# Optimization experiments

Measured on AMD Instinct MI355X. Metric: run time of the kernel, lower is better.

The kernel has to match this reference:

```python
import jax, jax.numpy as jnp
import numpy as np

NUM_USERS = 100_000
NUM_ITEMS = 50_000
DIM = 64
N_INTERACTIONS = 2_000_000  # symmetric nnz = 4M


def setup_inputs() -> dict:
    rng = np.random.default_rng(0)
    u = rng.integers(0, NUM_USERS, N_INTERACTIONS)
    it = rng.integers(0, NUM_ITEMS, N_INTERACTIONS) + NUM_USERS  # items offset by num_users
    rows = np.concatenate([u, it]).astype(np.int32)  # symmetric adjacency
    cols = np.concatenate([it, u]).astype(np.int32)
    n_nodes = NUM_USERS + NUM_ITEMS
    deg = np.bincount(rows, minlength=n_nodes).astype(np.float32)
    deg = np.maximum(deg, 1.0)
    # LightGCN symmetric normalization: A_hat[i,j] = 1/sqrt(deg_i * deg_j)
    vals = (1.0 / np.sqrt(deg[rows] * deg[cols])).astype(np.float32)

    key = jax.random.key(0)
    k1, k2 = jax.random.split(key)
    user_emb = jax.random.normal(k1, (NUM_USERS, DIM), jnp.float32) * 0.1
    item_emb = jax.random.normal(k2, (NUM_ITEMS, DIM), jnp.float32) * 0.1
    return {
        "user_emb": user_emb,
        "item_emb": item_emb,
        "rows": jnp.asarray(rows),
        "cols": jnp.asarray(cols),
        "vals": jnp.asarray(vals),
        "n_layers": 3,
    }


def reference(user_emb, item_emb, rows, cols, vals, n_layers):
    num_users = user_emb.shape[0]
    n_nodes = num_users + item_emb.shape[0]
    emb = jnp.concatenate([user_emb, item_emb], axis=0)  # [N, D]
    acc = emb
    cur = emb
    for _ in range(n_layers):
        # SpMM: cur = A_hat @ cur, via edge gather + weighted segment reduction
        msgs = vals[:, None] * cur[cols]  # [nnz, D]
        cur = jax.ops.segment_sum(msgs, rows, num_segments=n_nodes)
        acc = acc + cur
    all_emb = acc / (n_layers + 1)  # mean over [e0, e1, ..., eL]
    return all_emb[:num_users], all_emb[num_users:]
```

## Files before the change

kernel.cpp:

```cpp
#include <hip/hip_runtime.h>
#include <hip/hip_fp16.h>

#define D 64
#define NLAYERS 3
#define CHUNK 8192
#define RPB 256
#define NBMAX 640
#define NCHMAX 512
#define STAGE_CAP 8704

typedef float vfloat4 __attribute__((ext_vector_type(4)));

__global__ void init_concat(const float* __restrict__ ue, const float* __restrict__ ie,
                            const float* __restrict__ invsq,
                            __half* __restrict__ w0,
                            int n_user_elems, int n_total_elems) {
    int i4 = (blockIdx.x * blockDim.x + threadIdx.x) * 4;
    if (i4 >= n_total_elems) return;
    float4 v;
    if (i4 < n_user_elems) v = *(const float4*)(ue + i4);
    else                   v = *(const float4*)(ie + (i4 - n_user_elems));
    float isr = invsq[i4 >> 6];
    __half2 h01 = __floats2half2_rn(isr * v.x, isr * v.y);
    __half2 h23 = __floats2half2_rn(isr * v.z, isr * v.w);
    float2 packed;
    *(__half2*)&packed.x = h01;
    *(__half2*)&packed.y = h23;
    *(float2*)(w0 + i4) = packed;
}

__global__ void partition_edges(const int* __restrict__ rows, const int* __restrict__ cols,
                                int* __restrict__ gsorted, int* __restrict__ goff_c,
                                int nnz, int nb) {
    __shared__ int staged[CHUNK];
    __shared__ int cnt[NBMAX];
    __shared__ int cur[NBMAX];
    __shared__ int partial[256];
    int t = threadIdx.x;
    int base = blockIdx.x * CHUNK;

    for (int j = t; j <= nb; j += 256) cnt[j] = 0;
    __syncthreads();
    for (int k = 0; k < CHUNK; k += 256) {
        int e = base + k + t;
        if (e < nnz) atomicAdd(&cnt[rows[e] >> 8], 1);
    }
    __syncthreads();
    int i0 = t * 3, i1 = i0 + 1, i2 = i0 + 2;
    int v0 = (i0 < nb) ? cnt[i0] : 0;
    int v1 = (i1 < nb) ? cnt[i1] : 0;
    int v2 = (i2 < nb) ? cnt[i2] : 0;
    partial[t] = v0 + v1 + v2;
    __syncthreads();
    for (int off = 1; off < 256; off <<= 1) {
        int x = (t >= off) ? partial[t - off] : 0;
        __syncthreads();
        partial[t] += x;
        __syncthreads();
    }
    int excl = (t == 0) ? 0 : partial[t - 1];
    if (i0 <= nb) cnt[i0] = excl;
    if (i1 <= nb) cnt[i1] = excl + v0;
    if (i2 <= nb) cnt[i2] = excl + v0 + v1;
    __syncthreads();
    for (int j = t; j < nb; j += 256) cur[j] = cnt[j];
    __syncthreads();
    for (int k = 0; k < CHUNK; k += 256) {
        int e = base + k + t;
        if (e < nnz) {
            int r = rows[e];
            int pos = atomicAdd(&cur[r >> 8], 1);
            staged[pos] = ((r & 255) << 18) | cols[e];
        }
    }
    __syncthreads();
    int total = cnt[nb];
    for (int i = t; i < total; i += 256) gsorted[base + i] = staged[i];
    for (int j = t; j <= nb; j += 256) goff_c[blockIdx.x * (nb + 1) + j] = cnt[j];
}

__global__ void transpose_off(const int* __restrict__ goff_c, int* __restrict__ T,
                              int nch, int nbp1) {
    int c = blockIdx.x * 256 + threadIdx.x;
    int j = blockIdx.y;
    if (c < nch) T[j * nch + c] = goff_c[c * nbp1 + j];
}

__global__ void bucket_totals(const int* __restrict__ T, int* __restrict__ btot, int nch) {
    int b = blockIdx.x;
    int lane = threadIdx.x;
    int s = 0;
    for (int c = lane; c < nch; c += 64)
        s += T[(size_t)(b + 1) * nch + c] - T[(size_t)b * nch + c];
    for (int off = 32; off; off >>= 1) s += __shfl_down(s, off, 64);
    if (lane == 0) btot[b] = s;
}

__global__ void scan_buckets(const int* __restrict__ btot, int* __restrict__ bb,
                             int* __restrict__ rp, int nb, int n_nodes, int nnz) {
    __shared__ int partial[256];
    int t = threadIdx.x;
    int i0 = t * 3, i1 = i0 + 1, i2 = i0 + 2;
    int v0 = (i0 < nb) ? btot[i0] : 0;
    int v1 = (i1 < nb) ? btot[i1] : 0;
    int v2 = (i2 < nb) ? btot[i2] : 0;
    partial[t] = v0 + v1 + v2;
    __syncthreads();
    for (int off = 1; off < 256; off <<= 1) {
        int x = (t >= off) ? partial[t - off] : 0;
        __syncthreads();
        partial[t] += x;
        __syncthreads();
    }
    int excl = (t == 0) ? 0 : partial[t - 1];
    if (i0 <= nb) bb[i0] = excl;
    if (i1 <= nb) bb[i1] = excl + v0;
    if (i2 <= nb) bb[i2] = excl + v0 + v1;
    if (t == 0) rp[n_nodes] = nnz;
}

__global__ __launch_bounds__(256)
void csr_build_bucket(const int* __restrict__ T, const int* __restrict__ gsorted,
                      const int* __restrict__ bb,
                      int* __restrict__ rp, float* __restrict__ invsq,
                      int* __restrict__ ci, int nch, int n_nodes) {
    __shared__ int staged[STAGE_CAP];
    __shared__ int sbeg[NCHMAX];
    __shared__ int slen[NCHMAX];
    __shared__ int soff[NCHMAX];
    __shared__ int cnt[RPB];
    __shared__ int cursor[RPB];
    __shared__ int scanb[256];
    int t = threadIdx.x;
    int b = blockIdx.x;
    for (int j = t; j < nch; j += 256) {
        int s0 = T[(size_t)b * nch + j];
        int s1 = T[(size_t)(b + 1) * nch + j];
        sbeg[j] = s0;
        slen[j] = s1 - s0;
    }
    cnt[t] = 0;
    __syncthreads();
    int i0 = 2 * t, i1 = 2 * t + 1;
    int l0 = (i0 < nch) ? slen[i0] : 0;
    int l1 = (i1 < nch) ? slen[i1] : 0;
    scanb[t] = l0 + l1;
    __syncthreads();
    for (int off = 1; off < 256; off <<= 1) {
        int x = (t >= off) ? scanb[t - off] : 0;
        __syncthreads();
        scanb[t] += x;
        __syncthreads();
    }
    int texcl = scanb[t] - (l0 + l1);
    if (i0 < nch) soff[i0] = texcl;
    if (i1 < nch) soff[i1] = texcl + l0;
    int total = scanb[255];
    __syncthreads();

    int w = t >> 6, lane = t & 63;
    int sub = lane >> 4, l16 = lane & 15;
    bool fits = (total <= STAGE_CAP);
    if (fits) {
        for (int c = (w << 2) + sub; c < nch; c += 16) {
            const int* seg = gsorted + (size_t)c * CHUNK + sbeg[c];
            int L = slen[c], o = soff[c];
            for (int i = l16; i < L; i += 16) staged[o + i] = seg[i];
        }
        __syncthreads();
        for (int i = t; i < total; i += 256) atomicAdd(&cnt[staged[i] >> 18], 1);
    } else {
        for (int c = (w << 2) + sub; c < nch; c += 16) {
            const int* seg = gsorted + (size_t)c * CHUNK + sbeg[c];
            int L = slen[c];
            for (int i = l16; i < L; i += 16) atomicAdd(&cnt[seg[i] >> 18], 1);
        }
    }
    __syncthreads();
    int v = cnt[t];
    scanb[t] = v;
    __syncthreads();
    for (int off = 1; off < 256; off <<= 1) {
        int x = (t >= off) ? scanb[t - off] : 0;
        __syncthreads();
        scanb[t] += x;
        __syncthreads();
    }
    int excl = scanb[t] - v;
    int base = bb[b];
    int grow = (b << 8) + t;
    if (grow < n_nodes) {
        rp[grow] = base + excl;
        float d = (float)v;
        invsq[grow] = rsqrtf(d < 1.f ? 1.f : d);
    }
    cursor[t] = base + excl;
    __syncthreads();
    if (fits) {
        for (int i = t; i < total; i += 256) {
            int p = staged[i];
            int pos = atomicAdd(&cursor[p >> 18], 1);
            ci[pos] = p & 0x3FFFF;
        }
    } else {
        for (int c = (w << 2) + sub; c < nch; c += 16) {
            const int* seg = gsorted + (size_t)c * CHUNK + sbeg[c];
            int L = slen[c];
            for (int i = l16; i < L; i += 16) {
                int p = seg[i];
                int pos = atomicAdd(&cursor[p >> 18], 1);
                ci[pos] = p & 0x3FFFF;
            }
        }
    }
}

__global__ __launch_bounds__(256)
void spmm_gather(const int* __restrict__ rp, const int* __restrict__ ci,
                 const __half* __restrict__ xh, const float* __restrict__ invsq,
                 __half* __restrict__ ynext,
                 const __half* __restrict__ opA,
                 const float* __restrict__ e0,
                 float* __restrict__ outp,
                 int row_beg, int row_end, int last) {
    int wid  = row_beg + ((blockIdx.x * blockDim.x + threadIdx.x) >> 6);
    int lane = threadIdx.x & 63;
    if (wid >= row_end) return;
    int sub = lane >> 4;
    int d4  = (lane & 15) << 2;
    int beg = rp[wid], end = rp[wid + 1];
    float isr = invsq[wid];

    float4 b4;
    float2 q1, q2;
    if (last && sub == 0) {
        size_t o = ((size_t)wid << 6) + d4;
        b4 = *(const float4*)(e0 + o);
        q1 = *(const float2*)(opA + o);
        q2 = *(const float2*)(xh + o);
    }

    __half2 z = __floats2half2_rn(0.f, 0.f);
    __half2 a01 = z, a23 = z, b01 = z, b23 = z;
    __half2 c01 = z, c23 = z, d01 = z, d23 = z;
    int e = beg + sub;
    for (; e + 12 < end; e += 16) {
        int k0 = __builtin_nontemporal_load(ci + e);
        int k1 = __builtin_nontemporal_load(ci + e + 4);
        int k2 = __builtin_nontemporal_load(ci + e + 8);
        int k3 = __builtin_nontemporal_load(ci + e + 12);
        float2 r0 = *(const float2*)(xh + ((size_t)k0 << 6) + d4);
        float2 r1 = *(const float2*)(xh + ((size_t)k1 << 6) + d4);
        float2 r2 = *(const float2*)(xh + ((size_t)k2 << 6) + d4);
        float2 r3 = *(const float2*)(xh + ((size_t)k3 << 6) + d4);
        a01 = __hadd2(a01, *(__half2*)&r0.x); a23 = __hadd2(a23, *(__half2*)&r0.y);
        b01 = __hadd2(b01, *(__half2*)&r1.x); b23 = __hadd2(b23, *(__half2*)&r1.y);
        c01 = __hadd2(c01, *(__half2*)&r2.x); c23 = __hadd2(c23, *(__half2*)&r2.y);
        d01 = __hadd2(d01, *(__half2*)&r3.x); d23 = __hadd2(d23, *(__half2*)&r3.y);
    }
    for (; e + 4 < end; e += 8) {
        int k0 = __builtin_nontemporal_load(ci + e);
        int k1 = __builtin_nontemporal_load(ci + e + 4);
        float2 r0 = *(const float2*)(xh + ((size_t)k0 << 6) + d4);
        float2 r1 = *(const float2*)(xh + ((size_t)k1 << 6) + d4);
        a01 = __hadd2(a01, *(__half2*)&r0.x); a23 = __hadd2(a23, *(__half2*)&r0.y);
        b01 = __hadd2(b01, *(__half2*)&r1.x); b23 = __hadd2(b23, *(__half2*)&r1.y);
    }
    if (e < end) {
        int k0 = ci[e];
        float2 r0 = *(const float2*)(xh + ((size_t)k0 << 6) + d4);
        a01 = __hadd2(a01, *(__half2*)&r0.x); a23 = __hadd2(a23, *(__half2*)&r0.y);
    }
    float2 fa = __half22float2(a01), fb = __half22float2(b01);
    float2 fc = __half22float2(c01), fd = __half22float2(d01);
    float sx = (fa.x + fb.x) + (fc.x + fd.x);
    float sy = (fa.y + fb.y) + (fc.y + fd.y);
    fa = __half22float2(a23); fb = __half22float2(b23);
    fc = __half22float2(c23); fd = __half22float2(d23);
    float sz = (fa.x + fb.x) + (fc.x + fd.x);
    float sw = (fa.y + fb.y) + (fc.y + fd.y);
    sx += __shfl_xor(sx, 16, 64); sy += __shfl_xor(sy, 16, 64);
    sz += __shfl_xor(sz, 16, 64); sw += __shfl_xor(sw, 16, 64);
    sx += __shfl_xor(sx, 32, 64); sy += __shfl_xor(sy, 32, 64);
    sz += __shfl_xor(sz, 32, 64); sw += __shfl_xor(sw, 32, 64);

    if (sub == 0) {
        size_t o = ((size_t)wid << 6) + d4;
        float cx = isr * sx, cy = isr * sy, cz = isr * sz, cw = isr * sw;
        if (last) {
            float sd = 1.0f / isr;
            float2 f1a = __half22float2(*(__half2*)&q1.x);
            float2 f1b = __half22float2(*(__half2*)&q1.y);
            float2 f2a = __half22float2(*(__half2*)&q2.x);
            float2 f2b = __half22float2(*(__half2*)&q2.y);
            vfloat4 o4;
            o4.x = (b4.x + (f1a.x + f2a.x) * sd + cx) * 0.25f;
            o4.y = (b4.y + (f1a.y + f2a.y) * sd + cy) * 0.25f;
            o4.z = (b4.z + (f1b.x + f2b.x) * sd + cz) * 0.25f;
            o4.w = (b4.w + (f1b.y + f2b.y) * sd + cw) * 0.25f;
            __builtin_nontemporal_store(o4, (vfloat4*)(outp + o));
        } else {
            __half2 h01 = __floats2half2_rn(isr * cx, isr * cy);
            __half2 h23 = __floats2half2_rn(isr * cz, isr * cw);
            float2 packed;
            *(__half2*)&packed.x = h01;
            *(__half2*)&packed.y = h23;
            *(float2*)(ynext + o) = packed;
        }
    }
}

extern "C" void kernel_launch(void* const* d_in, const int* in_sizes, int n_in,
                              void* d_out, int out_size, void* d_ws, size_t ws_size,
                              hipStream_t stream) {
    const float* ue   = (const float*)d_in[0];
    const float* ie   = (const float*)d_in[1];
    const int*   rows = (const int*)d_in[2];
    const int*   cols = (const int*)d_in[3];

    const int n_user_elems  = in_sizes[0];
    const int n_total_elems = out_size;
    const int n_nodes       = n_total_elems / D;
    const int n_user        = n_user_elems / D;
    const int nnz           = in_sizes[2];

    const int nb  = (n_nodes + RPB - 1) / RPB;
    const int nch = (nnz + CHUNK - 1) / CHUNK;

    float* out = (float*)d_out;

    char* w = (char*)d_ws;
    __half* w0h    = (__half*)w; w += (size_t)n_total_elems * 2;
    __half* w1h    = (__half*)w; w += (size_t)n_total_elems * 2;
    int*   gsorted = (int*)w;    w += (size_t)nch * CHUNK * 4;
    int*   ci      = (int*)w;    w += (size_t)nnz * 4;
    float* invsq   = (float*)w;  w += (size_t)n_nodes * 4;
    int*   rp      = (int*)w;    w += ((size_t)n_nodes + 16) * 4;
    int*   goff_c  = (int*)w;    w += (size_t)nch * (nb + 1) * 4;
    int*   Tt      = (int*)w;    w += (size_t)(nb + 1) * nch * 4;
    int*   btot    = (int*)w;    w += (size_t)(nb + 16) * 4;
    int*   bb      = (int*)w;    w += (size_t)(nb + 16) * 4;

    partition_edges<<<nch, 256, 0, stream>>>(rows, cols, gsorted, goff_c, nnz, nb);
    dim3 tg((nch + 255) / 256, nb + 1);
    transpose_off<<<tg, 256, 0, stream>>>(goff_c, Tt, nch, nb + 1);
    bucket_totals<<<nb, 64, 0, stream>>>(Tt, btot, nch);
    scan_buckets<<<1, 256, 0, stream>>>(btot, bb, rp, nb, n_nodes, nnz);
    csr_build_bucket<<<nb, 256, 0, stream>>>(Tt, gsorted, bb, rp, invsq, ci, nch, n_nodes);

    const int elem_blocks = (n_total_elems / 4 + 255) / 256;
    init_concat<<<elem_blocks, 256, 0, stream>>>(ue, ie, invsq, w0h,
                                                 n_user_elems, n_total_elems);

    const float* e0u = ue;
    const float* e0i = ie - (size_t)n_user * D;
    __half* cur = w0h;
    __half* nxt = w1h;
    const int ublocks = (n_user * 64 + 255) / 256;
    const int iblocks = ((n_nodes - n_user) * 64 + 255) / 256;
    for (int l = 0; l < NLAYERS; ++l) {
        int last = (l == NLAYERS - 1);
        spmm_gather<<<ublocks, 256, 0, stream>>>(rp, ci, cur, invsq, nxt,
                                                 w1h, e0u, out, 0, n_user, last);
        spmm_gather<<<iblocks, 256, 0, stream>>>(rp, ci, cur, invsq, nxt,
                                                 w1h, e0i, out, n_user, n_nodes, last);
        __half* t = cur; cur = nxt; nxt = t;
    }
}
```

Measured before the change: 503.6 us.

## Pack row descriptors, merge SpMM launches, and order column indices by phase

Replaces the CSR row-pointer array and the separate invsq lookup with a packed int4 descriptor per row (begin, end, scale), so each wave makes one 16-byte load. The user and item SpMM launches merge into one launch per layer that picks the e0 base pointer per row. The CSR scatter now runs in 10 passes keyed on column range, so column indices within each row come out roughly sorted and gathers land in more local parts of the embedding table. The build kernel pays for this with repeated scans over the staged edges and extra barriers.

After: 605.3 us. 20.2% more time.

```diff
diff --git a/kernel.cpp b/kernel.cpp
--- a/kernel.cpp
+++ b/kernel.cpp
@@ -8,6 +8,7 @@
 #define NBMAX 640
 #define NCHMAX 512
 #define STAGE_CAP 8704
+#define NPHASE 10
 
 typedef float vfloat4 __attribute__((ext_vector_type(4)));
 
@@ -97,7 +98,7 @@
 }
 
 __global__ void scan_buckets(const int* __restrict__ btot, int* __restrict__ bb,
-                             int* __restrict__ rp, int nb, int n_nodes, int nnz) {
+                             int nb) {
     __shared__ int partial[256];
     int t = threadIdx.x;
     int i0 = t * 3, i1 = i0 + 1, i2 = i0 + 2;
@@ -116,13 +117,12 @@
     if (i0 <= nb) bb[i0] = excl;
     if (i1 <= nb) bb[i1] = excl + v0;
     if (i2 <= nb) bb[i2] = excl + v0 + v1;
-    if (t == 0) rp[n_nodes] = nnz;
 }
 
 __global__ __launch_bounds__(256)
 void csr_build_bucket(const int* __restrict__ T, const int* __restrict__ gsorted,
                       const int* __restrict__ bb,
-                      int* __restrict__ rp, float* __restrict__ invsq,
+                      int4* __restrict__ rdesc, float* __restrict__ invsq,
                       int* __restrict__ ci, int nch, int n_nodes) {
     __shared__ int staged[STAGE_CAP];
     __shared__ int sbeg[NCHMAX];
@@ -189,53 +189,75 @@
     int excl = scanb[t] - v;
     int base = bb[b];
     int grow = (b << 8) + t;
+    int rbeg = base + excl;
     if (grow < n_nodes) {
-        rp[grow] = base + excl;
         float d = (float)v;
-        invsq[grow] = rsqrtf(d < 1.f ? 1.f : d);
-    }
-    cursor[t] = base + excl;
+        float isr = rsqrtf(d < 1.f ? 1.f : d);
+        invsq[grow] = isr;
+        int4 rd;
+        rd.x = rbeg;
+        rd.y = rbeg + v;
+        rd.z = __float_as_int(isr);
+        rd.w = 0;
+        rdesc[grow] = rd;
+    }
+    cursor[t] = rbeg;
     __syncthreads();
     if (fits) {
-        for (int i = t; i < total; i += 256) {
-            int p = staged[i];
-            int pos = atomicAdd(&cursor[p >> 18], 1);
-            ci[pos] = p & 0x3FFFF;
+        for (int q = 0; q < NPHASE; ++q) {
+            for (int i = t; i < total; i += 256) {
+                int p = staged[i];
+                int c = p & 0x3FFFF;
+                if ((c >> 14) == q) {
+                    int pos = atomicAdd(&cursor[p >> 18], 1);
+                    ci[pos] = c;
+                }
+            }
+            __syncthreads();
         }
     } else {
-        for (int c = (w << 2) + sub; c < nch; c += 16) {
-            const int* seg = gsorted + (size_t)c * CHUNK + sbeg[c];
-            int L = slen[c];
-            for (int i = l16; i < L; i += 16) {
-                int p = seg[i];
-                int pos = atomicAdd(&cursor[p >> 18], 1);
-                ci[pos] = p & 0x3FFFF;
+        for (int q = 0; q < NPHASE; ++q) {
+            for (int c = (w << 2) + sub; c < nch; c += 16) {
+                const int* seg = gsorted + (size_t)c * CHUNK + sbeg[c];
+                int L = slen[c];
+                for (int i = l16; i < L; i += 16) {
+                    int p = seg[i];
+                    int cc = p & 0x3FFFF;
+                    if ((cc >> 14) == q) {
+                        int pos = atomicAdd(&cursor[p >> 18], 1);
+                        ci[pos] = cc;
+                    }
+                }
             }
+            __syncthreads();
         }
     }
 }
 
 __global__ __launch_bounds__(256)
-void spmm_gather(const int* __restrict__ rp, const int* __restrict__ ci,
-                 const __half* __restrict__ xh, const float* __restrict__ invsq,
+void spmm_gather(const int4* __restrict__ rdesc, const int* __restrict__ ci,
+                 const __half* __restrict__ xh,
                  __half* __restrict__ ynext,
                  const __half* __restrict__ opA,
-                 const float* __restrict__ e0,
+                 const float* __restrict__ ue, const float* __restrict__ ie,
                  float* __restrict__ outp,
-                 int row_beg, int row_end, int last) {
-    int wid  = row_beg + ((blockIdx.x * blockDim.x + threadIdx.x) >> 6);
+                 int n_user, int n_nodes, int last) {
+    int wid  = (blockIdx.x * blockDim.x + threadIdx.x) >> 6;
     int lane = threadIdx.x & 63;
-    if (wid >= row_end) return;
+    if (wid >= n_nodes) return;
     int sub = lane >> 4;
     int d4  = (lane & 15) << 2;
-    int beg = rp[wid], end = rp[wid + 1];
-    float isr = invsq[wid];
+    int4 rd = rdesc[wid];
+    int beg = rd.x, end = rd.y;
+    float isr = __int_as_float(rd.z);
 
     float4 b4;
     float2 q1, q2;
     if (last && sub == 0) {
         size_t o = ((size_t)wid << 6) + d4;
-        b4 = *(const float4*)(e0 + o);
+        const float* eb = (wid < n_user) ? (ue + o)
+                                         : (ie + o - ((size_t)n_user << 6));
+        b4 = *(const float4*)eb;
         q1 = *(const float2*)(opA + o);
         q2 = *(const float2*)(xh + o);
     }
@@ -335,7 +357,7 @@
     int*   gsorted = (int*)w;    w += (size_t)nch * CHUNK * 4;
     int*   ci      = (int*)w;    w += (size_t)nnz * 4;
     float* invsq   = (float*)w;  w += (size_t)n_nodes * 4;
-    int*   rp      = (int*)w;    w += ((size_t)n_nodes + 16) * 4;
+    int4*  rdesc   = (int4*)w;   w += ((size_t)n_nodes + 16) * 16;
     int*   goff_c  = (int*)w;    w += (size_t)nch * (nb + 1) * 4;
     int*   Tt      = (int*)w;    w += (size_t)(nb + 1) * nch * 4;
     int*   btot    = (int*)w;    w += (size_t)(nb + 16) * 4;
@@ -345,25 +367,21 @@
     dim3 tg((nch + 255) / 256, nb + 1);
     transpose_off<<<tg, 256, 0, stream>>>(goff_c, Tt, nch, nb + 1);
     bucket_totals<<<nb, 64, 0, stream>>>(Tt, btot, nch);
-    scan_buckets<<<1, 256, 0, stream>>>(btot, bb, rp, nb, n_nodes, nnz);
-    csr_build_bucket<<<nb, 256, 0, stream>>>(Tt, gsorted, bb, rp, invsq, ci, nch, n_nodes);
+    scan_buckets<<<1, 256, 0, stream>>>(btot, bb, nb);
+    csr_build_bucket<<<nb, 256, 0, stream>>>(Tt, gsorted, bb, rdesc, invsq, ci, nch, n_nodes);
 
     const int elem_blocks = (n_total_elems / 4 + 255) / 256;
     init_concat<<<elem_blocks, 256, 0, stream>>>(ue, ie, invsq, w0h,
                                                  n_user_elems, n_total_elems);
 
-    const float* e0u = ue;
-    const float* e0i = ie - (size_t)n_user * D;
     __half* cur = w0h;
     __half* nxt = w1h;
-    const int ublocks = (n_user * 64 + 255) / 256;
-    const int iblocks = ((n_nodes - n_user) * 64 + 255) / 256;
+    const int blocks = (n_nodes * 64 + 255) / 256;
     for (int l = 0; l < NLAYERS; ++l) {
         int last = (l == NLAYERS - 1);
-        spmm_gather<<<ublocks, 256, 0, stream>>>(rp, ci, cur, invsq, nxt,
-                                                 w1h, e0u, out, 0, n_user, last);
-        spmm_gather<<<iblocks, 256, 0, stream>>>(rp, ci, cur, invsq, nxt,
-                                                 w1h, e0i, out, n_user, n_nodes, last);
+        spmm_gather<<<blocks, 256, 0, stream>>>(rdesc, ci, cur, nxt,
+                                                w1h, ue, ie, out,
+                                                n_user, n_nodes, last);
         __half* t = cur; cur = nxt; nxt = t;
     }
 }
```
